# Performance work log

Measured on AMD Instinct MI355X. Metric: run time of the kernel, lower is better.

The kernel has to match this reference:

```python
import jax, jax.numpy as jnp
import numpy as np

FD, NH, SP, GS = 256, 4, 2, 80.0
E = FD // NH
SP3 = SP ** 3


def _bilinear(plane, uv):
    # plane: [B,C,H,W], uv: [B,N,2] in [0,1] -> [B,C,N] (align_corners=True style)
    B, C, H, W = plane.shape
    x = jnp.clip(uv[..., 0], 0.0, 1.0) * (W - 1)
    y = jnp.clip(uv[..., 1], 0.0, 1.0) * (H - 1)
    x0 = jnp.floor(x); y0 = jnp.floor(y)
    wx = (x - x0)[:, None, :]; wy = (y - y0)[:, None, :]
    x0i = x0.astype(jnp.int32); y0i = y0.astype(jnp.int32)
    x1i = jnp.minimum(x0i + 1, W - 1); y1i = jnp.minimum(y0i + 1, H - 1)
    g = jax.vmap(lambda pl, yy, xx: pl[:, yy, xx])  # per-batch gather -> [C,N]
    f00 = g(plane, y0i, x0i); f01 = g(plane, y0i, x1i)
    f10 = g(plane, y1i, x0i); f11 = g(plane, y1i, x1i)
    return (f00 * (1 - wy) * (1 - wx) + f01 * (1 - wy) * wx
            + f10 * wy * (1 - wx) + f11 * wy * wx)


def _triplane(p, c_xz, c_xy, c_yz):
    # p: [B,N,3] in [0,1] -> [B,N,FD]; sum of three plane samples (ConvONet style)
    px, py, pz = p[..., 0], p[..., 1], p[..., 2]
    f = (_bilinear(c_xz, jnp.stack([px, pz], -1))
         + _bilinear(c_xy, jnp.stack([px, py], -1))
         + _bilinear(c_yz, jnp.stack([py, pz], -1)))
    return jnp.swapaxes(f, 1, 2)


def setup_inputs() -> dict:
    key = jax.random.key(0)
    ks = jax.random.split(key, 10)
    bs, ns, H = 4, 1024, 128
    inp = {}
    inp['query_pos'] = jax.random.uniform(ks[0], (bs, ns, 3), dtype=jnp.float32)
    for i, nm in enumerate(['c_xz', 'c_xy', 'c_yz']):
        inp[nm] = jax.random.normal(ks[1 + i], (bs, FD, H, H), dtype=jnp.float32)

    def lin(k, fi, fo):  # xavier-uniform like torch init
        lim = (6.0 / (fi + fo)) ** 0.5
        return jax.random.uniform(k, (fi, fo), minval=-lim, maxval=lim, dtype=jnp.float32)

    # to_offset: small random weight (torch inits to 0; small noise exercises the path),
    # bias = normalized sp^3 anchor grid / grid_scale, tiled over heads (as in __init__)
    inp['w_off'] = 0.01 * jax.random.normal(ks[4], (FD, SP3 * NH * 3), dtype=jnp.float32)
    g = np.stack(np.meshgrid(np.arange(SP), np.arange(SP), np.arange(SP), indexing='ij'), axis=-1).astype(np.float32)
    gsc = (2.0 * g / max(SP - 1, 1) - 1.0) / GS  # [sp,sp,sp,3]
    inp['b_off'] = jnp.asarray(np.tile(gsc[:, :, :, None, :], (1, 1, 1, NH, 1)).reshape(-1))
    inp['w_q'] = lin(ks[5], FD, E); inp['b_q'] = jnp.zeros((E,), jnp.float32)
    inp['w_k'] = lin(ks[6], FD, E); inp['b_k'] = jnp.zeros((E,), jnp.float32)
    inp['w_v'] = lin(ks[7], FD, E); inp['b_v'] = jnp.zeros((E,), jnp.float32)
    inp['w_out'] = lin(ks[8], FD, FD); inp['b_out'] = jnp.zeros((FD,), jnp.float32)
    return inp


def reference(query_pos, c_xz, c_xy, c_yz, w_off, b_off, w_q, b_q, w_k, b_k, w_v, b_v, w_out, b_out):
    bs, ns, _ = query_pos.shape
    feature = _triplane(query_pos, c_xz, c_xy, c_yz)                 # [bs,ns,FD]
    off = (feature @ w_off + b_off).reshape(bs, ns, SP3, NH, 3)
    aux = off + query_pos[:, :, None, None, :]                        # [bs,ns,SP3,NH,3]
    aux_feat = _triplane(aux.reshape(bs, -1, 3), c_xz, c_xy, c_yz)
    aux_feat = aux_feat.reshape(bs * ns, SP3, NH, FD)
    k = jnp.swapaxes(aux_feat @ w_k + b_k, 1, 2)                      # [bn,NH,SP3,E]
    v = jnp.swapaxes(aux_feat @ w_v + b_v, 1, 2)
    # note: original does q / scale with scale = E**-0.5, i.e. q * sqrt(E)
    q = (feature @ w_q + b_q).reshape(bs * ns, 1, 1, E) * (E ** 0.5)
    q = jnp.broadcast_to(q, (bs * ns, NH, 1, E))
    sim = jnp.einsum('bnid,bnjd->bnij', q, k)                         # [bn,NH,1,SP3]
    attn = jax.nn.softmax(sim, axis=-1)                               # dropout = identity (eval)
    out = jnp.einsum('bnij,bnjd->bnid', attn, v)                      # [bn,NH,1,E]
    out = jnp.swapaxes(out, 1, 2).reshape(bs, ns, NH * E)
    return out @ w_out + b_out + feature
```

## Files before the change

### kernel.cpp

```cpp
#include <hip/hip_runtime.h>
#include <math.h>

#define FD   256
#define NH   4
#define SP3  8
#define NP   32
#define EDIM 64
#define H    128
#define NS   1024
#define BS   4
#define QT   8

#define TEX         (H*H)
#define BATCH_ELEMS (TEX*FD)
#define PAIR_B      2
#define PAIR_Q      (PAIR_B*NS)
#define PPLANE      (PAIR_B*BATCH_ELEMS)

#define WS_PLANES 0
#define WS_FEAT   (3*PPLANE)
#define WS_QK     (WS_FEAT + PAIR_Q*FD)
#define WS_AUX    (WS_QK   + PAIR_Q*FD)
#define WS_WF     (WS_AUX  + PAIR_Q*NP*3)

__global__ __launch_bounds__(256) void tpk2(
    const float* __restrict__ xz, const float* __restrict__ xy,
    const float* __restrict__ yz, float* __restrict__ dstAll, int b0)
{
  int bid = blockIdx.x;
  int tT = bid & 255; bid >>= 8;
  int bl = bid & 1;   bid >>= 1;
  int pl = bid;
  const float* src = pl == 0 ? xz : (pl == 1 ? xy : yz);
  float* dst = dstAll + (size_t)pl * PPLANE + (size_t)bl * BATCH_ELEMS;
  int b = b0 + bl;

  __shared__ float T[64 * 260];
  int lane = threadIdx.x & 63, w = threadIdx.x >> 6;
  int lrow = lane >> 4;
  int ltex = (lane & 15) << 2;

  const float* sbase = src + (size_t)b * FD * TEX + tT * 64;
  #pragma unroll
  for (int i = 0; i < 16; i++) {
    int c = i * 16 + w * 4 + lrow;
    float4 v = *(const float4*)(sbase + (size_t)c * TEX + ltex);
    T[(ltex + 0) * 260 + c] = v.x;
    T[(ltex + 1) * 260 + c] = v.y;
    T[(ltex + 2) * 260 + c] = v.z;
    T[(ltex + 3) * 260 + c] = v.w;
  }
  __syncthreads();
  #pragma unroll
  for (int i = 0; i < 16; i++) {
    int t = w * 16 + i;
    float4 v = *(const float4*)(&T[t * 260 + lane * 4]);
    *(float4*)(dst + (size_t)(tT * 64 + t) * FD + lane * 4) = v;
  }
}

__device__ __forceinline__ float sample_plane(const float* __restrict__ p,
                                              float u, float v) {
  float x = fminf(fmaxf(u, 0.f), 1.f) * (float)(H - 1);
  float y = fminf(fmaxf(v, 0.f), 1.f) * (float)(H - 1);
  float xf = floorf(x), yf = floorf(y);
  int x0 = (int)xf, y0 = (int)yf;
  float wx = x - xf, wy = y - yf;
  int dx = (x0 < H - 1) ? FD : 0;
  int dy = (y0 < H - 1) ? H * FD : 0;
  int i00 = (y0 * H + x0) * FD;
  float f00 = p[i00], f01 = p[i00 + dx], f10 = p[i00 + dy], f11 = p[i00 + dy + dx];
  float a = f00 + wx * (f01 - f00);
  float b = f10 + wx * (f11 - f10);
  return a + wy * (b - a);
}

__device__ __forceinline__ void setup_samp(int* si, float* sw, float u, float v) {
  float x = fminf(fmaxf(u, 0.f), 1.f) * (float)(H - 1);
  float y = fminf(fmaxf(v, 0.f), 1.f) * (float)(H - 1);
  float xf = floorf(x), yf = floorf(y);
  int x0 = (int)xf, y0 = (int)yf;
  float wx = x - xf, wy = y - yf;
  si[0] = (y0 * H + x0) * FD;
  si[1] = (x0 < H - 1) ? FD : 0;
  si[2] = (y0 < H - 1) ? H * FD : 0;
  sw[0] = (1.f - wy) * (1.f - wx);
  sw[1] = (1.f - wy) * wx;
  sw[2] = wy * (1.f - wx);
  sw[3] = wy * wx;
}

__device__ __forceinline__ float bil(const float* __restrict__ p,
                                     const int* si, const float* sw) {
  int i00 = si[0], dx = si[1], dy = si[2];
  float f00 = p[i00], f01 = p[i00 + dx], f10 = p[i00 + dy], f11 = p[i00 + dy + dx];
  return fmaf(sw[0], f00, fmaf(sw[1], f01, fmaf(sw[2], f10, sw[3] * f11)));
}

__global__ __launch_bounds__(256) void featk(
    const float* __restrict__ qpos, const float* __restrict__ planesT,
    const float* __restrict__ w_off, const float* __restrict__ b_off,
    const float* __restrict__ w_q, const float* __restrict__ b_q,
    const float* __restrict__ w_k,
    float* __restrict__ feat, float* __restrict__ aux, float* __restrict__ qk,
    int b0)
{
  const int tid = threadIdx.x;
  const int q0l = blockIdx.x * QT;
  const int bl = q0l >> 10;
  __shared__ float s_feat[QT * 260];
  __shared__ float s_q[QT * 68];

  const float* Pxz = planesT + 0 * (size_t)PPLANE + (size_t)bl * BATCH_ELEMS + tid;
  const float* Pxy = planesT + 1 * (size_t)PPLANE + (size_t)bl * BATCH_ELEMS + tid;
  const float* Pyz = planesT + 2 * (size_t)PPLANE + (size_t)bl * BATCH_ELEMS + tid;

  for (int qs = 0; qs < QT; qs++) {
    size_t qg = (size_t)b0 * NS + q0l + qs;
    float px = qpos[qg * 3 + 0], py = qpos[qg * 3 + 1], pz = qpos[qg * 3 + 2];
    float f = sample_plane(Pxz, px, pz) + sample_plane(Pxy, px, py)
            + sample_plane(Pyz, py, pz);
    s_feat[qs * 260 + tid] = f;
    feat[(size_t)(q0l + qs) * FD + tid] = f;
  }
  __syncthreads();

  if (tid < 192) {
    int half = tid / 96, j = tid - half * 96;
    float acc[4];
    float bj = b_off[j];
    #pragma unroll
    for (int k = 0; k < 4; k++) acc[k] = bj;
    for (int c = 0; c < FD; c++) {
      float wv = w_off[c * 96 + j];
      #pragma unroll
      for (int k = 0; k < 4; k++)
        acc[k] = fmaf(s_feat[(half * 4 + k) * 260 + c], wv, acc[k]);
    }
    int d = j % 3;
    #pragma unroll
    for (int k = 0; k < 4; k++) {
      int qs = half * 4 + k;
      size_t qg = (size_t)b0 * NS + q0l + qs;
      aux[(size_t)(q0l + qs) * 96 + j] = acc[k] + qpos[qg * 3 + d];
    }
  }
  {
    int e = tid & 63, g = tid >> 6;
    #pragma unroll
    for (int k = 0; k < 2; k++) {
      int qs = g * 2 + k;
      float a = b_q[e];
      for (int c = 0; c < FD; c++)
        a = fmaf(s_feat[qs * 260 + c], w_q[c * EDIM + e], a);
      s_q[qs * 68 + e] = a * 8.0f;
    }
  }
  __syncthreads();
  {
    float acc[QT];
    #pragma unroll
    for (int qs = 0; qs < QT; qs++) acc[qs] = 0.f;
    const float4* wk4 = reinterpret_cast<const float4*>(w_k + (size_t)tid * EDIM);
    for (int e4 = 0; e4 < EDIM / 4; e4++) {
      float4 wv = wk4[e4];
      int e = e4 * 4;
      #pragma unroll
      for (int qs = 0; qs < QT; qs++) {
        acc[qs] = fmaf(s_q[qs * 68 + e + 0], wv.x, acc[qs]);
        acc[qs] = fmaf(s_q[qs * 68 + e + 1], wv.y, acc[qs]);
        acc[qs] = fmaf(s_q[qs * 68 + e + 2], wv.z, acc[qs]);
        acc[qs] = fmaf(s_q[qs * 68 + e + 3], wv.w, acc[qs]);
      }
    }
    #pragma unroll
    for (int qs = 0; qs < QT; qs++)
      qk[(size_t)(q0l + qs) * FD + tid] = acc[qs];
  }
}

__global__ __launch_bounds__(256) void attnk(
    const float* __restrict__ planesT, const float* __restrict__ aux,
    const float* __restrict__ qk, float* __restrict__ wf)
{
  const int tid = threadIdx.x, lane = tid & 63, wid = tid >> 6;
  const int q = blockIdx.x;
  const int bl = q >> 10;

  __shared__ int   s_si[96][3];
  __shared__ float s_sw[96][4];
  __shared__ float s_af[NP * 260];
  __shared__ float s_part[NP][4];
  __shared__ float s_attn[NP];

  const float* Pxz = planesT + (size_t)bl * BATCH_ELEMS + tid;
  const float* Pxy = Pxz + (size_t)PPLANE;
  const float* Pyz = Pxy + (size_t)PPLANE;

  if (tid < 96) {
    int p = tid / 3, pl = tid - p * 3;
    float ax = aux[(size_t)q * 96 + p * 3 + 0];
    float ay = aux[(size_t)q * 96 + p * 3 + 1];
    float az = aux[(size_t)q * 96 + p * 3 + 2];
    float u = (pl == 2) ? ay : ax;
    float v = (pl == 1) ? ay : az;
    setup_samp(s_si[tid], s_sw[tid], u, v);
  }
  float qkc = qk[(size_t)q * FD + tid];
  __syncthreads();

  #pragma unroll 4
  for (int p = 0; p < NP; p++) {
    float v = bil(Pxz, s_si[p * 3 + 0], s_sw[p * 3 + 0])
            + bil(Pxy, s_si[p * 3 + 1], s_sw[p * 3 + 1])
            + bil(Pyz, s_si[p * 3 + 2], s_sw[p * 3 + 2]);
    s_af[p * 260 + tid] = v;
    float t = qkc * v;
    #pragma unroll
    for (int o = 32; o >= 1; o >>= 1) t += __shfl_xor(t, o, 64);
    if (lane == 0) s_part[p][wid] = t;
  }
  __syncthreads();

  if (tid < NH) {
    float sim[SP3], m = -1e30f;
    #pragma unroll
    for (int j = 0; j < SP3; j++) {
      int p = j * NH + tid;
      float s = s_part[p][0] + s_part[p][1] + s_part[p][2] + s_part[p][3];
      sim[j] = s; m = fmaxf(m, s);
    }
    float sum = 0.f, e_[SP3];
    #pragma unroll
    for (int j = 0; j < SP3; j++) { e_[j] = __expf(sim[j] - m); sum += e_[j]; }
    float inv = 1.0f / sum;
    #pragma unroll
    for (int j = 0; j < SP3; j++) s_attn[j * NH + tid] = e_[j] * inv;
  }
  __syncthreads();

  float w0 = 0.f, w1 = 0.f, w2 = 0.f, w3 = 0.f;
  #pragma unroll
  for (int j = 0; j < SP3; j++) {
    w0 = fmaf(s_attn[j * NH + 0], s_af[(j * NH + 0) * 260 + tid], w0);
    w1 = fmaf(s_attn[j * NH + 1], s_af[(j * NH + 1) * 260 + tid], w1);
    w2 = fmaf(s_attn[j * NH + 2], s_af[(j * NH + 2) * 260 + tid], w2);
    w3 = fmaf(s_attn[j * NH + 3], s_af[(j * NH + 3) * 260 + tid], w3);
  }
  wf[((size_t)q * NH + 0) * FD + tid] = w0;
  wf[((size_t)q * NH + 1) * FD + tid] = w1;
  wf[((size_t)q * NH + 2) * FD + tid] = w2;
  wf[((size_t)q * NH + 3) * FD + tid] = w3;
}

__global__ __launch_bounds__(256) void epik(
    const float* __restrict__ wf, const float* __restrict__ feat,
    const float* __restrict__ w_v, const float* __restrict__ b_v,
    const float* __restrict__ w_out, const float* __restrict__ b_out,
    float* __restrict__ out, int b0)
{
  const int tid = threadIdx.x;
  const int q0l = blockIdx.x * QT;
  __shared__ float s_wv[FD * EDIM];
  __shared__ float s_o[QT * 257];

  {
    const float4* src4 = (const float4*)w_v;
    float4* dst4 = (float4*)s_wv;
    #pragma unroll
    for (int i = 0; i < (FD * EDIM / 4) / 256; i++)
      dst4[tid + 256 * i] = src4[tid + 256 * i];
  }
  __syncthreads();

  {
    int h = tid >> 6, e = tid & 63;
    float acc[QT];
    float bv = b_v[e];
    #pragma unroll
    for (int qs = 0; qs < QT; qs++) acc[qs] = bv;
    const float* wrow = wf + ((size_t)q0l * NH + h) * FD;
    for (int c = 0; c < FD; c++) {
      float wv = s_wv[c * EDIM + e];
      #pragma unroll
      for (int qs = 0; qs < QT; qs++)
        acc[qs] = fmaf(wrow[(size_t)qs * NH * FD + c], wv, acc[qs]);
    }
    #pragma unroll
    for (int qs = 0; qs < QT; qs++) s_o[qs * 257 + h * EDIM + e] = acc[qs];
  }
  __syncthreads();

  {
    float r[QT];
    float bo = b_out[tid];
    #pragma unroll
    for (int qs = 0; qs < QT; qs++) r[qs] = bo;
    for (int c = 0; c < FD; c++) {
      float wv = w_out[(size_t)c * FD + tid];
      #pragma unroll
      for (int qs = 0; qs < QT; qs++)
        r[qs] = fmaf(s_o[qs * 257 + c], wv, r[qs]);
    }
    #pragma unroll
    for (int qs = 0; qs < QT; qs++)
      out[((size_t)b0 * NS + q0l + qs) * FD + tid]
          = r[qs] + feat[(size_t)(q0l + qs) * FD + tid];
  }
}

extern "C" void kernel_launch(void* const* d_in, const int* in_sizes, int n_in,
                              void* d_out, int out_size, void* d_ws, size_t ws_size,
                              hipStream_t stream) {
  const float* qp    = (const float*)d_in[0];
  const float* cxz   = (const float*)d_in[1];
  const float* cxy   = (const float*)d_in[2];
  const float* cyz   = (const float*)d_in[3];
  const float* w_off = (const float*)d_in[4];
  const float* b_off = (const float*)d_in[5];
  const float* w_q   = (const float*)d_in[6];
  const float* b_q   = (const float*)d_in[7];
  const float* w_k   = (const float*)d_in[8];
  const float* b_k   = (const float*)d_in[9];   (void)b_k;
  const float* w_v   = (const float*)d_in[10];
  const float* b_v   = (const float*)d_in[11];
  const float* w_out = (const float*)d_in[12];
  const float* b_out = (const float*)d_in[13];
  float* out = (float*)d_out;
  (void)in_sizes; (void)n_in; (void)out_size; (void)ws_size;

  float* ws      = (float*)d_ws;
  float* planesT = ws + WS_PLANES;
  float* feat    = ws + WS_FEAT;
  float* qk      = ws + WS_QK;
  float* aux     = ws + WS_AUX;
  float* wf      = ws + WS_WF;

  for (int pair = 0; pair < BS / PAIR_B; ++pair) {
    int b0 = pair * PAIR_B;
    hipLaunchKernelGGL(tpk2, dim3(3 * PAIR_B * 256), dim3(256), 0, stream,
                       cxz, cxy, cyz, planesT, b0);
    hipLaunchKernelGGL(featk, dim3(PAIR_Q / QT), dim3(256), 0, stream,
                       qp, planesT, w_off, b_off, w_q, b_q, w_k,
                       feat, aux, qk, b0);
    hipLaunchKernelGGL(attnk, dim3(PAIR_Q), dim3(256), 0, stream,
                       planesT, aux, qk, wf);
    hipLaunchKernelGGL(epik, dim3(PAIR_Q / QT), dim3(256), 0, stream,
                       wf, feat, w_v, b_v, w_out, b_out, out, b0);
  }
}
```

Measured before the change: 552.0 us.

## Vectorize attention gathers per wave, double query tile, drop w_v shared staging

The attention kernel now has each wave handle 8 sample points, with each lane loading float4 channel groups. Aux features stay in registers instead of a large shared buffer, and the per-head weighted sums are reduced through a small shared array. The query tile for the feature and epilogue kernels grows from 8 to 16, which halves the block count and reuses each weight load across more queries. The epilogue no longer stages w_v in 64KB of shared memory and reads it from global or cache directly. This trades shared-memory footprint and occupancy limits for more registers per thread and fewer, larger blocks.

After: 751.6 us. 36.2% more time.

```diff
diff --git a/kernel.cpp b/kernel.cpp
--- a/kernel.cpp
+++ b/kernel.cpp
@@ -9,7 +9,7 @@
 #define H    128
 #define NS   1024
 #define BS   4
-#define QT   8
+#define QT   16
 
 #define TEX         (H*H)
 #define BATCH_ELEMS (TEX*FD)
@@ -90,13 +90,6 @@
   sw[3] = wy * wx;
 }
 
-__device__ __forceinline__ float bil(const float* __restrict__ p,
-                                     const int* si, const float* sw) {
-  int i00 = si[0], dx = si[1], dy = si[2];
-  float f00 = p[i00], f01 = p[i00 + dx], f10 = p[i00 + dy], f11 = p[i00 + dy + dx];
-  return fmaf(sw[0], f00, fmaf(sw[1], f01, fmaf(sw[2], f10, sw[3] * f11)));
-}
-
 __global__ __launch_bounds__(256) void featk(
     const float* __restrict__ qpos, const float* __restrict__ planesT,
     const float* __restrict__ w_off, const float* __restrict__ b_off,
@@ -127,20 +120,20 @@
 
   if (tid < 192) {
     int half = tid / 96, j = tid - half * 96;
-    float acc[4];
+    float acc[8];
     float bj = b_off[j];
     #pragma unroll
-    for (int k = 0; k < 4; k++) acc[k] = bj;
+    for (int k = 0; k < 8; k++) acc[k] = bj;
     for (int c = 0; c < FD; c++) {
       float wv = w_off[c * 96 + j];
       #pragma unroll
-      for (int k = 0; k < 4; k++)
-        acc[k] = fmaf(s_feat[(half * 4 + k) * 260 + c], wv, acc[k]);
+      for (int k = 0; k < 8; k++)
+        acc[k] = fmaf(s_feat[(half * 8 + k) * 260 + c], wv, acc[k]);
     }
     int d = j % 3;
     #pragma unroll
-    for (int k = 0; k < 4; k++) {
-      int qs = half * 4 + k;
+    for (int k = 0; k < 8; k++) {
+      int qs = half * 8 + k;
       size_t qg = (size_t)b0 * NS + q0l + qs;
       aux[(size_t)(q0l + qs) * 96 + j] = acc[k] + qpos[qg * 3 + d];
     }
@@ -148,8 +141,8 @@
   {
     int e = tid & 63, g = tid >> 6;
     #pragma unroll
-    for (int k = 0; k < 2; k++) {
-      int qs = g * 2 + k;
+    for (int k = 0; k < 4; k++) {
+      int qs = g * 4 + k;
       float a = b_q[e];
       for (int c = 0; c < FD; c++)
         a = fmaf(s_feat[qs * 260 + c], w_q[c * EDIM + e], a);
@@ -179,23 +172,24 @@
   }
 }
 
-__global__ __launch_bounds__(256) void attnk(
+__global__ __launch_bounds__(256, 4) void attnk(
     const float* __restrict__ planesT, const float* __restrict__ aux,
     const float* __restrict__ qk, float* __restrict__ wf)
 {
-  const int tid = threadIdx.x, lane = tid & 63, wid = tid >> 6;
+  const int tid = threadIdx.x, lane = tid & 63, w = tid >> 6;
   const int q = blockIdx.x;
   const int bl = q >> 10;
+  const int c4 = lane * 4;
 
   __shared__ int   s_si[96][3];
   __shared__ float s_sw[96][4];
-  __shared__ float s_af[NP * 260];
-  __shared__ float s_part[NP][4];
+  __shared__ float s_sim[NP];
   __shared__ float s_attn[NP];
-
-  const float* Pxz = planesT + (size_t)bl * BATCH_ELEMS + tid;
-  const float* Pxy = Pxz + (size_t)PPLANE;
-  const float* Pyz = Pxy + (size_t)PPLANE;
+  __shared__ float4 s_wp[16 * 64];
+
+  const float* P0 = planesT + 0 * (size_t)PPLANE + (size_t)bl * BATCH_ELEMS + c4;
+  const float* P1 = planesT + 1 * (size_t)PPLANE + (size_t)bl * BATCH_ELEMS + c4;
+  const float* P2 = planesT + 2 * (size_t)PPLANE + (size_t)bl * BATCH_ELEMS + c4;
 
   if (tid < 96) {
     int p = tid / 3, pl = tid - p * 3;
@@ -206,30 +200,43 @@
     float v = (pl == 1) ? ay : az;
     setup_samp(s_si[tid], s_sw[tid], u, v);
   }
-  float qkc = qk[(size_t)q * FD + tid];
-  __syncthreads();
-
-  #pragma unroll 4
-  for (int p = 0; p < NP; p++) {
-    float v = bil(Pxz, s_si[p * 3 + 0], s_sw[p * 3 + 0])
-            + bil(Pxy, s_si[p * 3 + 1], s_sw[p * 3 + 1])
-            + bil(Pyz, s_si[p * 3 + 2], s_sw[p * 3 + 2]);
-    s_af[p * 260 + tid] = v;
-    float t = qkc * v;
+  float4 qk4 = *(const float4*)(qk + (size_t)q * FD + c4);
+  __syncthreads();
+
+  float4 afr[8];
+  #pragma unroll 2
+  for (int k = 0; k < 8; k++) {
+    int p = w * 8 + k;
+    float4 a; a.x = 0.f; a.y = 0.f; a.z = 0.f; a.w = 0.f;
+    #pragma unroll
+    for (int pl = 0; pl < 3; pl++) {
+      const float* P = pl == 0 ? P0 : (pl == 1 ? P1 : P2);
+      int i00 = s_si[p * 3 + pl][0];
+      int dxo = s_si[p * 3 + pl][1];
+      int dyo = s_si[p * 3 + pl][2];
+      float w0 = s_sw[p * 3 + pl][0], w1 = s_sw[p * 3 + pl][1];
+      float w2 = s_sw[p * 3 + pl][2], w3 = s_sw[p * 3 + pl][3];
+      float4 f00 = *(const float4*)(P + i00);
+      float4 f01 = *(const float4*)(P + i00 + dxo);
+      float4 f10 = *(const float4*)(P + i00 + dyo);
+      float4 f11 = *(const float4*)(P + i00 + dyo + dxo);
+      a.x = fmaf(w0, f00.x, fmaf(w1, f01.x, fmaf(w2, f10.x, fmaf(w3, f11.x, a.x))));
+      a.y = fmaf(w0, f00.y, fmaf(w1, f01.y, fmaf(w2, f10.y, fmaf(w3, f11.y, a.y))));
+      a.z = fmaf(w0, f00.z, fmaf(w1, f01.z, fmaf(w2, f10.z, fmaf(w3, f11.z, a.z))));
+      a.w = fmaf(w0, f00.w, fmaf(w1, f01.w, fmaf(w2, f10.w, fmaf(w3, f11.w, a.w))));
+    }
+    afr[k] = a;
+    float t = fmaf(qk4.x, a.x, fmaf(qk4.y, a.y, fmaf(qk4.z, a.z, qk4.w * a.w)));
     #pragma unroll
     for (int o = 32; o >= 1; o >>= 1) t += __shfl_xor(t, o, 64);
-    if (lane == 0) s_part[p][wid] = t;
+    if (lane == 0) s_sim[p] = t;
   }
   __syncthreads();
 
   if (tid < NH) {
     float sim[SP3], m = -1e30f;
     #pragma unroll
-    for (int j = 0; j < SP3; j++) {
-      int p = j * NH + tid;
-      float s = s_part[p][0] + s_part[p][1] + s_part[p][2] + s_part[p][3];
-      sim[j] = s; m = fmaxf(m, s);
-    }
+    for (int j = 0; j < SP3; j++) { sim[j] = s_sim[j * NH + tid]; m = fmaxf(m, sim[j]); }
     float sum = 0.f, e_[SP3];
     #pragma unroll
     for (int j = 0; j < SP3; j++) { e_[j] = __expf(sim[j] - m); sum += e_[j]; }
@@ -239,18 +246,33 @@
   }
   __syncthreads();
 
-  float w0 = 0.f, w1 = 0.f, w2 = 0.f, w3 = 0.f;
-  #pragma unroll
-  for (int j = 0; j < SP3; j++) {
-    w0 = fmaf(s_attn[j * NH + 0], s_af[(j * NH + 0) * 260 + tid], w0);
-    w1 = fmaf(s_attn[j * NH + 1], s_af[(j * NH + 1) * 260 + tid], w1);
-    w2 = fmaf(s_attn[j * NH + 2], s_af[(j * NH + 2) * 260 + tid], w2);
-    w3 = fmaf(s_attn[j * NH + 3], s_af[(j * NH + 3) * 260 + tid], w3);
-  }
-  wf[((size_t)q * NH + 0) * FD + tid] = w0;
-  wf[((size_t)q * NH + 1) * FD + tid] = w1;
-  wf[((size_t)q * NH + 2) * FD + tid] = w2;
-  wf[((size_t)q * NH + 3) * FD + tid] = w3;
+  float4 acc[NH];
+  #pragma unroll
+  for (int h = 0; h < NH; h++) { acc[h].x = 0.f; acc[h].y = 0.f; acc[h].z = 0.f; acc[h].w = 0.f; }
+  #pragma unroll
+  for (int k = 0; k < 8; k++) {
+    int p = w * 8 + k, h = p & 3;
+    float a = s_attn[p];
+    acc[h].x = fmaf(a, afr[k].x, acc[h].x);
+    acc[h].y = fmaf(a, afr[k].y, acc[h].y);
+    acc[h].z = fmaf(a, afr[k].z, acc[h].z);
+    acc[h].w = fmaf(a, afr[k].w, acc[h].w);
+  }
+  #pragma unroll
+  for (int h = 0; h < NH; h++) s_wp[(w * 4 + h) * 64 + lane] = acc[h];
+  __syncthreads();
+
+  {
+    float4 r0 = s_wp[(0 * 4 + w) * 64 + lane];
+    float4 r1 = s_wp[(1 * 4 + w) * 64 + lane];
+    float4 r2 = s_wp[(2 * 4 + w) * 64 + lane];
+    float4 r3 = s_wp[(3 * 4 + w) * 64 + lane];
+    float4 r; r.x = r0.x + r1.x + r2.x + r3.x;
+    r.y = r0.y + r1.y + r2.y + r3.y;
+    r.z = r0.z + r1.z + r2.z + r3.z;
+    r.w = r0.w + r1.w + r2.w + r3.w;
+    *(float4*)(wf + ((size_t)q * NH + w) * FD + c4) = r;
+  }
 }
 
 __global__ __launch_bounds__(256) void epik(
@@ -261,17 +283,7 @@
 {
   const int tid = threadIdx.x;
   const int q0l = blockIdx.x * QT;
-  __shared__ float s_wv[FD * EDIM];
   __shared__ float s_o[QT * 257];
-
-  {
-    const float4* src4 = (const float4*)w_v;
-    float4* dst4 = (float4*)s_wv;
-    #pragma unroll
-    for (int i = 0; i < (FD * EDIM / 4) / 256; i++)
-      dst4[tid + 256 * i] = src4[tid + 256 * i];
-  }
-  __syncthreads();
 
   {
     int h = tid >> 6, e = tid & 63;
@@ -281,7 +293,7 @@
     for (int qs = 0; qs < QT; qs++) acc[qs] = bv;
     const float* wrow = wf + ((size_t)q0l * NH + h) * FD;
     for (int c = 0; c < FD; c++) {
-      float wv = s_wv[c * EDIM + e];
+      float wv = w_v[c * EDIM + e];
       #pragma unroll
       for (int qs = 0; qs < QT; qs++)
         acc[qs] = fmaf(wrow[(size_t)qs * NH * FD + c], wv, acc[qs]);
```
